# Kernel tuning notes

Measured on AMD Instinct MI355X. Metric: run time of the kernel, lower is better.

## Reference

```python
import jax, jax.numpy as jnp
import numpy as np

D_MODEL = 1024
N_LAYERS = 2
D_STATE = 16
D_CONV = 4
D_INNER = 2 * D_MODEL          # mamba expand=2
DT_RANK = 64                   # ceil(d_model/16)
EPS = 1e-5


def rmsnorm(x, w, eps=EPS):
    return x * jax.lax.rsqrt(jnp.mean(x * x, axis=-1, keepdims=True) + eps) * w


def silu(x):
    return x * jax.nn.sigmoid(x)


def selective_scan(u, dt, A, B, C, Dp):
    # u, dt: (b,l,d)  A: (d,n)  B,C: (b,l,n)  Dp: (d,)
    b, l, d = u.shape
    n = A.shape[1]

    def step(h, inp):
        u_t, dt_t, B_t, C_t = inp          # (b,d),(b,d),(b,n),(b,n)
        dA = jnp.exp(dt_t[..., None] * A)  # (b,d,n)
        h = dA * h + (dt_t * u_t)[..., None] * B_t[:, None, :]
        y = jnp.einsum('bdn,bn->bd', h, C_t)
        return h, y

    h0 = jnp.zeros((b, d, n), u.dtype)
    xs = (u.transpose(1, 0, 2), dt.transpose(1, 0, 2),
          B.transpose(1, 0, 2), C.transpose(1, 0, 2))
    _, ys = jax.lax.scan(step, h0, xs)
    return ys.transpose(1, 0, 2) + u * Dp


def mamba_mixer(x, in_w, conv_w, conv_b, xp_w, dt_w, dt_b, A_log, Dp, out_w):
    b, l, _ = x.shape
    xz = jnp.einsum('bld,ed->ble', x, in_w)        # (b,l,2*d_inner)
    xi, z = jnp.split(xz, 2, axis=-1)
    # depthwise causal conv1d, kernel D_CONV
    xp = jnp.pad(xi, ((0, 0), (D_CONV - 1, 0), (0, 0)))
    xc = conv_b + sum(xp[:, k:k + l, :] * conv_w[:, k] for k in range(D_CONV))
    xc = silu(xc)
    dbc = jnp.einsum('bld,ed->ble', xc, xp_w)      # (b,l,dt_rank+2n)
    dt_low = dbc[..., :DT_RANK]
    Bm = dbc[..., DT_RANK:DT_RANK + D_STATE]
    Cm = dbc[..., DT_RANK + D_STATE:]
    dt = jax.nn.softplus(jnp.einsum('blr,dr->bld', dt_low, dt_w) + dt_b)
    A = -jnp.exp(A_log)
    y = selective_scan(xc, dt, A, Bm, Cm, Dp)
    y = y * silu(z)
    return jnp.einsum('bld,od->blo', y, out_w)


def setup_inputs() -> dict:
    key = jax.random.key(0)
    ks = jax.random.split(key, 8)
    s = 0.02
    hidden_states = jax.random.normal(ks[0], (1, 2048, D_MODEL), jnp.float32)
    norm_w = jnp.ones((N_LAYERS, D_MODEL), jnp.float32)
    in_proj_w = jax.random.normal(ks[1], (N_LAYERS, 2 * D_INNER, D_MODEL), jnp.float32) * s
    conv_w = jax.random.normal(ks[2], (N_LAYERS, D_INNER, D_CONV), jnp.float32) * 0.2
    conv_b = jnp.zeros((N_LAYERS, D_INNER), jnp.float32)
    x_proj_w = jax.random.normal(ks[3], (N_LAYERS, DT_RANK + 2 * D_STATE, D_INNER), jnp.float32) * s
    dt_proj_w = jax.random.normal(ks[4], (N_LAYERS, D_INNER, DT_RANK), jnp.float32) * (DT_RANK ** -0.5)
    # softplus^{-1}(0.01) ~= -4.6 (mamba dt bias init regime)
    dt_proj_b = jnp.full((N_LAYERS, D_INNER), -4.6, jnp.float32) + \
        jax.random.normal(ks[5], (N_LAYERS, D_INNER), jnp.float32) * 0.1
    A_log = jnp.log(jnp.broadcast_to(
        jnp.arange(1, D_STATE + 1, dtype=jnp.float32), (N_LAYERS, D_INNER, D_STATE)))
    D_param = jnp.ones((N_LAYERS, D_INNER), jnp.float32)
    out_proj_w = jax.random.normal(ks[6], (N_LAYERS, D_MODEL, D_INNER), jnp.float32) * s
    norm_f_w = jnp.ones((D_MODEL,), jnp.float32)
    return {
        'hidden_states': hidden_states, 'norm_w': norm_w, 'in_proj_w': in_proj_w,
        'conv_w': conv_w, 'conv_b': conv_b, 'x_proj_w': x_proj_w,
        'dt_proj_w': dt_proj_w, 'dt_proj_b': dt_proj_b, 'A_log': A_log,
        'D_param': D_param, 'out_proj_w': out_proj_w, 'norm_f_w': norm_f_w,
    }


def reference(hidden_states, norm_w, in_proj_w, conv_w, conv_b, x_proj_w,
              dt_proj_w, dt_proj_b, A_log, D_param, out_proj_w, norm_f_w):
    h = hidden_states
    residual = None
    for i in range(N_LAYERS):
        # fused add + RMSNorm (prenorm): residual accumulates the stream
        residual = h if residual is None else h + residual
        hn = rmsnorm(residual, norm_w[i])
        h = mamba_mixer(hn, in_proj_w[i], conv_w[i], conv_b[i], x_proj_w[i],
                        dt_proj_w[i], dt_proj_b[i], A_log[i], D_param[i], out_proj_w[i])
    # final fused add + RMSNorm (prenorm=False)
    return rmsnorm(h + residual, norm_f_w)
```

## Files before the change

### kernel.cpp

```cpp
#include <hip/hip_runtime.h>
#include <math.h>

#define D_MODEL 1024
#define D_INNER 2048
#define DPROJ   96
#define DT_RANK 64
#define NSTATE  16
#define SEQ     2048
#define CL      16
#define NCH     (SEQ/CL)
#define SCAN_SEGS 4
#define SCAN_CPS  (NCH / SCAN_SEGS)
#define LOG2E   1.44269504088896340736f
#define TDC     ((size_t)SEQ * D_MODEL)

typedef unsigned short ushort_t;
typedef short v8s __attribute__((ext_vector_type(8)));
typedef unsigned short u8s __attribute__((ext_vector_type(8)));
typedef float v4f __attribute__((ext_vector_type(4)));
typedef __attribute__((address_space(3))) unsigned int as3_u32;
typedef __attribute__((address_space(1))) unsigned int as1_u32;

__device__ __forceinline__ float silu_f(float x) { return x / (1.f + expf(-x)); }

__device__ __forceinline__ ushort_t f2bf(float f) {
  union { float f; unsigned u; } x; x.f = f;
  unsigned r = x.u + 0x7fffu + ((x.u >> 16) & 1u);
  return (ushort_t)(r >> 16);
}
__device__ __forceinline__ float bf2f(ushort_t b) {
  union { unsigned u; float f; } x; x.u = ((unsigned)b) << 16; return x.f;
}

__device__ __forceinline__ void gl_lds16(const ushort_t* g, ushort_t* l) {
  __builtin_amdgcn_global_load_lds((const as1_u32*)g, (as3_u32*)l, 16, 0, 0);
}

__global__ __launch_bounds__(256) void addrms_kernel(
    const float* __restrict__ a, const ushort_t* __restrict__ p4,
    const float* __restrict__ b,
    const float* __restrict__ w, float* __restrict__ res_out,
    float* __restrict__ xnf, ushort_t* __restrict__ xnb) {
  int t = blockIdx.x;
  int tid = threadIdx.x;
  float v[4];
  float ss = 0.f;
#pragma unroll
  for (int j = 0; j < 4; ++j) {
    int dcol = tid + j * 256;
    size_t off = (size_t)t * D_MODEL + dcol;
    float x;
    if (p4) {
      x = bf2f(p4[off]) + bf2f(p4[off + TDC]) +
          bf2f(p4[off + 2 * TDC]) + bf2f(p4[off + 3 * TDC]);
    } else {
      x = a[off];
    }
    if (b) x += b[off];
    v[j] = x;
    ss += x * x;
  }
#pragma unroll
  for (int off = 32; off > 0; off >>= 1) ss += __shfl_down(ss, off);
  __shared__ float red[4];
  __shared__ float rmsv;
  int wid = tid >> 6, lane = tid & 63;
  if (lane == 0) red[wid] = ss;
  __syncthreads();
  if (tid == 0) {
    float s = red[0] + red[1] + red[2] + red[3];
    rmsv = rsqrtf(s / (float)D_MODEL + 1e-5f);
  }
  __syncthreads();
  float r = rmsv;
#pragma unroll
  for (int j = 0; j < 4; ++j) {
    int dcol = tid + j * 256;
    if (res_out) res_out[(size_t)t * D_MODEL + dcol] = v[j];
    float xn = v[j] * r * w[dcol];
    if (xnf) xnf[(size_t)t * D_MODEL + dcol] = xn;
    if (xnb) xnb[(size_t)t * D_MODEL + dcol] = f2bf(xn);
  }
}

__global__ __launch_bounds__(256) void f2bf_all_kernel(
    const float* __restrict__ s0, ushort_t* __restrict__ d0, int n0,
    const float* __restrict__ s1, ushort_t* __restrict__ d1, int n1,
    const float* __restrict__ s2, ushort_t* __restrict__ d2, int n2,
    const float* __restrict__ s3, ushort_t* __restrict__ d3, int n3) {
  int j = blockIdx.x * 256 + threadIdx.x;
  const float* s; ushort_t* d;
  if (j < n0) { s = s0; d = d0; }
  else {
    j -= n0;
    if (j < n1) { s = s1; d = d1; }
    else {
      j -= n1;
      if (j < n2) { s = s2; d = d2; }
      else {
        j -= n2;
        if (j >= n3) return;
        s = s3; d = d3;
      }
    }
  }
  float4 v = ((const float4*)s)[j];
  ushort4 o;
  o.x = f2bf(v.x); o.y = f2bf(v.y); o.z = f2bf(v.z); o.w = f2bf(v.w);
  ((ushort4*)d)[j] = o;
}

template <int SPLITK, bool CLAMPN, int EPI>
__global__ __launch_bounds__(256) void gemm_bt(
    const ushort_t* __restrict__ A, const ushort_t* __restrict__ B,
    void* __restrict__ Cv, const float* __restrict__ bias,
    const ushort_t* __restrict__ upack,
    int M, int N, int K, int lda, int ldb, int ldc) {
  __shared__ ushort_t As[2][128 * 32];
  __shared__ ushort_t Bs[2][128 * 32];
  int tid = threadIdx.x;

  int gx = gridDim.x, gy = gridDim.y;
  int nwg = gx * gy * gridDim.z;
  int phys = blockIdx.x + gx * (blockIdx.y + gy * blockIdx.z);
  int q = nwg >> 3, r = nwg & 7;
  int xcd = phys & 7, idx8 = phys >> 3;
  int lbid = (xcd < r ? xcd * (q + 1) : r * (q + 1) + (xcd - r) * q) + idx8;
  int bx = lbid % gx, by = (lbid / gx) % gy, bz = lbid / (gx * gy);

  int bm = by * 128;
  int bn = bx * 128;
  int kchunk = K / SPLITK;
  int k0 = bz * kchunk;
  int nk = kchunk / 32;

  int lane = tid & 63, wid = tid >> 6;
  int wr = wid >> 1, wc = wid & 1;
  int lr = lane & 15;
  int ko = (lane >> 4) * 8;

  int rs0 = wid * 16 + (lane >> 2);
  int segc = (lane & 3) * 8;

  auto stage = [&](int buf, int kt) {
#pragma unroll
    for (int s = 0; s < 2; ++s) {
      int r2 = s * 64 + rs0;
      int cc = kt + segc;
      gl_lds16(A + (size_t)(bm + r2) * lda + cc, &As[buf][s * 2048 + wid * 512]);
      int bc = bn + r2;
      if (CLAMPN) bc = min(bc, N - 1);
      gl_lds16(B + (size_t)bc * ldb + cc, &Bs[buf][s * 2048 + wid * 512]);
    }
  };

  v4f acc[4][4] = {};

  stage(0, k0);
  __syncthreads();
  int cur = 0;
  for (int it = 0; it < nk; ++it) {
    if (it + 1 < nk) stage(cur ^ 1, k0 + (it + 1) * 32);
    v8s a[4], b[4];
#pragma unroll
    for (int m = 0; m < 4; ++m)
      a[m] = *(const v8s*)&As[cur][(wr * 64 + m * 16 + lr) * 32 + ko];
#pragma unroll
    for (int n = 0; n < 4; ++n)
      b[n] = *(const v8s*)&Bs[cur][(wc * 64 + n * 16 + lr) * 32 + ko];
#pragma unroll
    for (int m = 0; m < 4; ++m)
#pragma unroll
      for (int n = 0; n < 4; ++n)
        acc[m][n] = __builtin_amdgcn_mfma_f32_16x16x32_bf16(a[m], b[n], acc[m][n], 0, 0, 0);
    __syncthreads();
    cur ^= 1;
  }

  float* Cf = (float*)Cv;
  ushort_t* Cb = (ushort_t*)Cv;
  unsigned* Cu = (unsigned*)Cv;
  size_t zoff = (SPLITK > 1) ? (size_t)bz * (size_t)M * (size_t)ldc : 0;

#pragma unroll
  for (int m = 0; m < 4; ++m) {
#pragma unroll
    for (int n = 0; n < 4; ++n) {
      int gc = bn + wc * 64 + n * 16 + lr;
      if (gc >= N) continue;
      int gr0 = bm + wr * 64 + m * 16 + (lane >> 4) * 4;
      float bv = (EPI == 1 || EPI == 3) ? bias[gc] : 0.f;
#pragma unroll
      for (int j = 0; j < 4; ++j) {
        float val = acc[m][n][j];
        size_t idx = zoff + (size_t)(gr0 + j) * ldc + gc;
        if (EPI == 0) {
          Cf[idx] = val;
        } else if (EPI == 1) {
          float x = val + bv;
          x = fmaxf(x, 0.f) + log1pf(expf(-fabsf(x)));
          Cb[idx] = f2bf(x);
        } else if (EPI == 2) {
          Cb[idx] = f2bf(val);
        } else {
          float x = val + bv;
          x = fmaxf(x, 0.f) + log1pf(expf(-fabsf(x)));
          Cu[idx] = (unsigned)f2bf(x) | ((unsigned)upack[idx] << 16);
        }
      }
    }
  }
}

__global__ __launch_bounds__(256) void convxproj_kernel(
    const ushort_t* __restrict__ xzb, const float* __restrict__ cw,
    const float* __restrict__ cb, const ushort_t* __restrict__ Bw,
    ushort_t* __restrict__ xcb, ushort_t* __restrict__ pkb) {
  __shared__ ushort_t As[128][136];
  __shared__ ushort_t Bs[2][128 * 32];
  int tid = threadIdx.x;
  int bm = blockIdx.y * 128;
  int c0s = blockIdx.z * 128;
  int k0 = c0s;

  {
    int quad = tid & 31;
    int tg = tid >> 5;
    int cc = c0s + quad * 4;
    int tbase = bm + tg * 16;
    float4 cbv = *(const float4*)&cb[cc];
    float4 wv[4];
#pragma unroll
    for (int i = 0; i < 4; ++i) wv[i] = *(const float4*)&cw[(cc + i) * 4];
    float rw[4][4];
#pragma unroll
    for (int p = 0; p < 3; ++p) {
      int ts = tbase - 3 + p;
      if (ts < 0) {
        rw[p][0] = rw[p][1] = rw[p][2] = rw[p][3] = 0.f;
      } else {
        ushort4 x = *(const ushort4*)&xzb[(size_t)ts * 4096 + cc];
        rw[p][0] = bf2f(x.x); rw[p][1] = bf2f(x.y);
        rw[p][2] = bf2f(x.z); rw[p][3] = bf2f(x.w);
      }
    }
#pragma unroll
    for (int j = 0; j < 16; ++j) {
      int t = tbase + j;
      {
        ushort4 x = *(const ushort4*)&xzb[(size_t)t * 4096 + cc];
        rw[(3 + j) & 3][0] = bf2f(x.x); rw[(3 + j) & 3][1] = bf2f(x.y);
        rw[(3 + j) & 3][2] = bf2f(x.z); rw[(3 + j) & 3][3] = bf2f(x.w);
      }
      float acc[4] = {cbv.x, cbv.y, cbv.z, cbv.w};
#pragma unroll
      for (int k = 0; k < 4; ++k) {
#pragma unroll
        for (int i = 0; i < 4; ++i)
          acc[i] = fmaf(rw[(j + k) & 3][i], ((const float*)&wv[i])[k], acc[i]);
      }
      ushort4 o;
      o.x = f2bf(silu_f(acc[0]));
      o.y = f2bf(silu_f(acc[1]));
      o.z = f2bf(silu_f(acc[2]));
      o.w = f2bf(silu_f(acc[3]));
      *(ushort4*)&As[tg * 16 + j][quad * 4] = o;
      *(ushort4*)&xcb[(size_t)t * D_INNER + cc] = o;
    }
  }

  int lane = tid & 63, wid = tid >> 6;
  int wr = wid >> 1, wc = wid & 1;
  int lr = lane & 15;
  int ko = (lane >> 4) * 8;
  int rs0 = wid * 16 + (lane >> 2);
  int segc = (lane & 3) * 8;

  auto stageB = [&](int buf, int it) {
#pragma unroll
    for (int s = 0; s < 2; ++s) {
      int r2 = s * 64 + rs0;
      int bc = min(r2, DPROJ - 1);
      int cc2 = k0 + it * 32 + segc;
      gl_lds16(Bw + (size_t)bc * D_INNER + cc2, &Bs[buf][s * 2048 + wid * 512]);
    }
  };

  v4f acc[4][4] = {};
  stageB(0, 0);
  __syncthreads();
  int cur = 0;
  for (int it = 0; it < 4; ++it) {
    if (it + 1 < 4) stageB(cur ^ 1, it + 1);
    v8s a[4], b[4];
#pragma unroll
    for (int m = 0; m < 4; ++m)
      a[m] = *(const v8s*)&As[wr * 64 + m * 16 + lr][it * 32 + ko];
#pragma unroll
    for (int n = 0; n < 4; ++n)
      b[n] = *(const v8s*)&Bs[cur][(wc * 64 + n * 16 + lr) * 32 + ko];
#pragma unroll
    for (int m = 0; m < 4; ++m)
#pragma unroll
      for (int n = 0; n < 4; ++n)
        acc[m][n] = __builtin_amdgcn_mfma_f32_16x16x32_bf16(a[m], b[n], acc[m][n], 0, 0, 0);
    __syncthreads();
    cur ^= 1;
  }

  size_t zoff = (size_t)blockIdx.z * (size_t)SEQ * DPROJ;
#pragma unroll
  for (int m = 0; m < 4; ++m) {
#pragma unroll
    for (int n = 0; n < 4; ++n) {
      int gc = wc * 64 + n * 16 + lr;
      if (gc >= DPROJ) continue;
      int gr0 = bm + wr * 64 + m * 16 + (lane >> 4) * 4;
#pragma unroll
      for (int j = 0; j < 4; ++j)
        pkb[zoff + (size_t)(gr0 + j) * DPROJ + gc] = f2bf(acc[m][n][j]);
    }
  }
}

__global__ __launch_bounds__(256) void reduceNb_kernel(
    const ushort_t* __restrict__ part, ushort_t* __restrict__ outb,
    int sz, int nparts) {
  int idx = blockIdx.x * 256 + threadIdx.x;
  if (idx >= sz) return;
  float s = 0.f;
  for (int p = 0; p < nparts; ++p) s += bf2f(part[idx + (size_t)p * sz]);
  outb[idx] = f2bf(s);
}

__global__ __launch_bounds__(256) void scan_passA_kernel(
    const unsigned* __restrict__ dtu, const ushort_t* __restrict__ dbcb,
    const float* __restrict__ A_log,
    ushort_t* __restrict__ aprodb, ushort_t* __restrict__ hendb) {
  __shared__ float Bsh[CL][16];
  int c = blockIdx.x;
  int d = blockIdx.y * 256 + threadIdx.x;
  int t0 = c * CL;
  {
    int j = threadIdx.x;
    if (j < CL * 4) {
      int r = j >> 2, col = (j & 3) * 4;
      ushort4 v = *(const ushort4*)&dbcb[(size_t)(t0 + r) * DPROJ + DT_RANK + col];
      Bsh[r][col]     = bf2f(v.x);
      Bsh[r][col + 1] = bf2f(v.y);
      Bsh[r][col + 2] = bf2f(v.z);
      Bsh[r][col + 3] = bf2f(v.w);
    }
  }
  float Av[NSTATE], h[NSTATE], ap[NSTATE];
#pragma unroll
  for (int n = 0; n < NSTATE; ++n) {
    Av[n] = -expf(A_log[(size_t)d * NSTATE + n]) * LOG2E;
    h[n] = 0.f;
    ap[n] = 1.f;
  }
  __syncthreads();
#pragma unroll 2
  for (int tt = 0; tt < CL; ++tt) {
    unsigned p = dtu[(size_t)(t0 + tt) * D_INNER + d];
    float dtv = bf2f((ushort_t)(p & 0xffffu));
    float uv  = bf2f((ushort_t)(p >> 16));
    float du = dtv * uv;
#pragma unroll
    for (int n = 0; n < NSTATE; ++n) {
      float dA = exp2f(dtv * Av[n]);
      h[n] = fmaf(dA, h[n], du * Bsh[tt][n]);
      ap[n] *= dA;
    }
  }
  size_t base = ((size_t)c * D_INNER + d) * NSTATE;
  u8s oa, ob, ha, hb;
#pragma unroll
  for (int n = 0; n < 8; ++n) {
    oa[n] = f2bf(ap[n]);     ob[n] = f2bf(ap[n + 8]);
    ha[n] = f2bf(h[n]);      hb[n] = f2bf(h[n + 8]);
  }
  *(u8s*)&aprodb[base] = oa;     *(u8s*)&aprodb[base + 8] = ob;
  *(u8s*)&hendb[base]  = ha;     *(u8s*)&hendb[base + 8]  = hb;
}

__global__ __launch_bounds__(256) void scan_passB_kernel(
    const ushort_t* __restrict__ aprodb, ushort_t* __restrict__ hendb) {
  int tid = threadIdx.x;
  int lane = tid & 63;
  int wave = tid >> 6;
  int seg = lane >> 4;
  int chain = blockIdx.x * 64 + wave * 16 + (lane & 15);
  const size_t stride = (size_t)D_INNER * NSTATE;
  float a[SCAN_CPS], e[SCAN_CPS];
  float P = 1.f, E = 0.f;
  int c0 = seg * SCAN_CPS;
#pragma unroll
  for (int j = 0; j < SCAN_CPS; ++j) {
    a[j] = bf2f(aprodb[(size_t)(c0 + j) * stride + chain]);
    e[j] = bf2f(hendb[(size_t)(c0 + j) * stride + chain]);
    E = fmaf(a[j], E, e[j]);
    P *= a[j];
  }
#pragma unroll
  for (int dstep = 1; dstep < SCAN_SEGS; dstep <<= 1) {
    float Pp = __shfl_up(P, dstep * 16);
    float Ep = __shfl_up(E, dstep * 16);
    if (seg >= dstep) { E = fmaf(P, Ep, E); P *= Pp; }
  }
  float Ex = __shfl_up(E, 16);
  if (seg == 0) Ex = 0.f;
  float h = Ex;
#pragma unroll
  for (int j = 0; j < SCAN_CPS; ++j) {
    hendb[(size_t)(c0 + j) * stride + chain] = f2bf(h);
    h = fmaf(a[j], h, e[j]);
  }
}

__global__ __launch_bounds__(256) void scan_passC_kernel(
    const unsigned* __restrict__ dtu, const ushort_t* __restrict__ dbcb,
    const float* __restrict__ A_log, const float* __restrict__ Dp,
    const ushort_t* __restrict__ xzb, const ushort_t* __restrict__ hinb,
    ushort_t* __restrict__ yb) {
  __shared__ float BCsh[CL][32];
  int c = blockIdx.x;
  int d = blockIdx.y * 256 + threadIdx.x;
  int t0 = c * CL;
  {
    int j = threadIdx.x;
    if (j < CL * 8) {
      int r = j >> 3, col = (j & 7) * 4;
      ushort4 v = *(const ushort4*)&dbcb[(size_t)(t0 + r) * DPROJ + DT_RANK + col];
      BCsh[r][col]     = bf2f(v.x);
      BCsh[r][col + 1] = bf2f(v.y);
      BCsh[r][col + 2] = bf2f(v.z);
      BCsh[r][col + 3] = bf2f(v.w);
    }
  }
  float Av[NSTATE], h[NSTATE];
  size_t base = ((size_t)c * D_INNER + d) * NSTATE;
  u8s h0 = *(const u8s*)&hinb[base];
  u8s h1 = *(const u8s*)&hinb[base + 8];
#pragma unroll
  for (int n = 0; n < NSTATE; ++n) {
    Av[n] = -expf(A_log[(size_t)d * NSTATE + n]) * LOG2E;
    h[n] = (n < 8) ? bf2f(h0[n & 7]) : bf2f(h1[n & 7]);
  }
  float Dv = Dp[d];
  __syncthreads();
#pragma unroll 2
  for (int tt = 0; tt < CL; ++tt) {
    unsigned p = dtu[(size_t)(t0 + tt) * D_INNER + d];
    float dtv = bf2f((ushort_t)(p & 0xffffu));
    float uv  = bf2f((ushort_t)(p >> 16));
    float du = dtv * uv;
    float yv = 0.f;
#pragma unroll
    for (int n = 0; n < NSTATE; ++n) {
      float dA = exp2f(dtv * Av[n]);
      h[n] = fmaf(dA, h[n], du * BCsh[tt][n]);
      yv = fmaf(h[n], BCsh[tt][16 + n], yv);
    }
    float zv = bf2f(xzb[(size_t)(t0 + tt) * 4096 + D_INNER + d]);
    yb[(size_t)(t0 + tt) * D_INNER + d] = f2bf((yv + uv * Dv) * silu_f(zv));
  }
}

extern "C" void kernel_launch(void* const* d_in, const int* in_sizes, int n_in,
                              void* d_out, int out_size, void* d_ws, size_t ws_size,
                              hipStream_t stream) {
  const float* h_in   = (const float*)d_in[0];
  const float* norm_w = (const float*)d_in[1];
  const float* in_w   = (const float*)d_in[2];
  const float* conv_w = (const float*)d_in[3];
  const float* conv_b = (const float*)d_in[4];
  const float* xp_w   = (const float*)d_in[5];
  const float* dt_w   = (const float*)d_in[6];
  const float* dt_b   = (const float*)d_in[7];
  const float* A_log  = (const float*)d_in[8];
  const float* Dp     = (const float*)d_in[9];
  const float* out_w  = (const float*)d_in[10];
  const float* normf  = (const float*)d_in[11];
  float* out = (float*)d_out;

  float* ws = (float*)d_ws;
  const size_t TD = (size_t)SEQ * D_MODEL;
  const size_t TI = (size_t)SEQ * D_INNER;
  const size_t ST = (size_t)NCH * D_INNER * NSTATE;
  const size_t DB = (size_t)SEQ * DPROJ;
  const size_t INW = (size_t)2 * D_INNER * D_MODEL;
  const size_t XPW = (size_t)DPROJ * D_INNER;
  const size_t DTW = (size_t)D_INNER * DT_RANK;
  const size_t OUW = (size_t)D_MODEL * D_INNER;

  float* res = ws; ws += TD;
  ushort_t* pkb = (ushort_t*)ws; ws += 2 * TD;
  unsigned* dtu = (unsigned*)ws; ws += TI;
  ushort_t* us = (ushort_t*)ws;
  ushort_t* aprodb = us;  us += ST;
  ushort_t* hendb  = us;  us += ST;
  ushort_t* hnb  = us;    us += TD;
  ushort_t* xzb  = us;    us += 2 * TI;
  ushort_t* xcb  = us;    us += TI;
  ushort_t* ybf  = us;    us += TI;
  ushort_t* dbcb = us;    us += DB;
  ushort_t* inwb = us;    us += 2 * INW;
  ushort_t* xpwb = us;    us += 2 * XPW;
  ushort_t* dtwb = us;    us += 2 * DTW;
  ushort_t* ouwb = us;    us += 2 * OUW;

  {
    int n0 = (int)(2 * INW / 4), n1 = (int)(2 * XPW / 4);
    int n2 = (int)(2 * DTW / 4), n3 = (int)(2 * OUW / 4);
    int tot = n0 + n1 + n2 + n3;
    f2bf_all_kernel<<<(tot + 255) / 256, 256, 0, stream>>>(
        in_w, inwb, n0, xp_w, xpwb, n1, dt_w, dtwb, n2, out_w, ouwb, n3);
  }

  for (int i = 0; i < 2; ++i) {
    addrms_kernel<<<SEQ, 256, 0, stream>>>(
        h_in, i == 0 ? nullptr : pkb,
        i == 0 ? nullptr : res,
        norm_w + (size_t)i * D_MODEL, res, nullptr, hnb);
    gemm_bt<1, false, 2><<<dim3(32, 16, 1), 256, 0, stream>>>(
        hnb, inwb + (size_t)i * INW, xzb, nullptr, nullptr,
        SEQ, 2 * D_INNER, D_MODEL, D_MODEL, D_MODEL, 2 * D_INNER);
    convxproj_kernel<<<dim3(1, 16, 16), 256, 0, stream>>>(
        xzb, conv_w + (size_t)i * D_INNER * 4, conv_b + (size_t)i * D_INNER,
        xpwb + (size_t)i * XPW, xcb, pkb);
    reduceNb_kernel<<<(DB + 255) / 256, 256, 0, stream>>>(pkb, dbcb, (int)DB, 16);
    gemm_bt<1, false, 3><<<dim3(16, 16, 1), 256, 0, stream>>>(
        dbcb, dtwb + (size_t)i * DTW, dtu, dt_b + (size_t)i * D_INNER, xcb,
        SEQ, D_INNER, DT_RANK, DPROJ, DT_RANK, D_INNER);
    scan_passA_kernel<<<dim3(NCH, D_INNER / 256), 256, 0, stream>>>(
        dtu, dbcb, A_log + (size_t)i * D_INNER * NSTATE, aprodb, hendb);
    scan_passB_kernel<<<(D_INNER * NSTATE) / 64, 256, 0, stream>>>(aprodb, hendb);
    scan_passC_kernel<<<dim3(NCH, D_INNER / 256), 256, 0, stream>>>(
        dtu, dbcb, A_log + (size_t)i * D_INNER * NSTATE,
        Dp + (size_t)i * D_INNER, xzb, hendb, ybf);
    gemm_bt<4, false, 2><<<dim3(8, 16, 4), 256, 0, stream>>>(
        ybf, ouwb + (size_t)i * OUW, pkb, nullptr, nullptr,
        SEQ, D_MODEL, D_INNER, D_INNER, D_INNER, D_MODEL);
  }
  addrms_kernel<<<SEQ, 256, 0, stream>>>(
      h_in, pkb, res, normf, nullptr, out, nullptr);
}
```

Baseline: 340.3 us.

## Split-K in_proj and out_proj GEMMs, reduce partials in consumers

The in_proj GEMM becomes split-K=2, writing two bf16 partial buffers that the conv and scan-C kernels sum when they read them. The out_proj GEMM goes from split-K 4 to 8, with addrms summing a variable number of partials. The dt GEMM no longer packs u with dt, so the scan kernels read dt and xc from separate arrays. This raises workgroup counts to fill more CUs, at the cost of extra partial-buffer traffic, a wider workspace, and an extra bf16 rounding per partial.

```diff
diff --git a/kernel.cpp b/kernel.cpp
--- a/kernel.cpp
+++ b/kernel.cpp
@@ -13,6 +13,7 @@
 #define SCAN_CPS  (NCH / SCAN_SEGS)
 #define LOG2E   1.44269504088896340736f
 #define TDC     ((size_t)SEQ * D_MODEL)
+#define XZP1    ((size_t)SEQ * 4096)
 
 typedef unsigned short ushort_t;
 typedef short v8s __attribute__((ext_vector_type(8)));
@@ -37,7 +38,7 @@
 }
 
 __global__ __launch_bounds__(256) void addrms_kernel(
-    const float* __restrict__ a, const ushort_t* __restrict__ p4,
+    const float* __restrict__ a, const ushort_t* __restrict__ pN, int nparts,
     const float* __restrict__ b,
     const float* __restrict__ w, float* __restrict__ res_out,
     float* __restrict__ xnf, ushort_t* __restrict__ xnb) {
@@ -50,9 +51,9 @@
     int dcol = tid + j * 256;
     size_t off = (size_t)t * D_MODEL + dcol;
     float x;
-    if (p4) {
-      x = bf2f(p4[off]) + bf2f(p4[off + TDC]) +
-          bf2f(p4[off + 2 * TDC]) + bf2f(p4[off + 3 * TDC]);
+    if (pN) {
+      x = 0.f;
+      for (int p = 0; p < nparts; ++p) x += bf2f(pN[off + (size_t)p * TDC]);
     } else {
       x = a[off];
     }
@@ -114,7 +115,6 @@
 __global__ __launch_bounds__(256) void gemm_bt(
     const ushort_t* __restrict__ A, const ushort_t* __restrict__ B,
     void* __restrict__ Cv, const float* __restrict__ bias,
-    const ushort_t* __restrict__ upack,
     int M, int N, int K, int lda, int ldb, int ldc) {
   __shared__ ushort_t As[2][128 * 32];
   __shared__ ushort_t Bs[2][128 * 32];
@@ -179,7 +179,6 @@
 
   float* Cf = (float*)Cv;
   ushort_t* Cb = (ushort_t*)Cv;
-  unsigned* Cu = (unsigned*)Cv;
   size_t zoff = (SPLITK > 1) ? (size_t)bz * (size_t)M * (size_t)ldc : 0;
 
 #pragma unroll
@@ -189,7 +188,7 @@
       int gc = bn + wc * 64 + n * 16 + lr;
       if (gc >= N) continue;
       int gr0 = bm + wr * 64 + m * 16 + (lane >> 4) * 4;
-      float bv = (EPI == 1 || EPI == 3) ? bias[gc] : 0.f;
+      float bv = (EPI == 1) ? bias[gc] : 0.f;
 #pragma unroll
       for (int j = 0; j < 4; ++j) {
         float val = acc[m][n][j];
@@ -200,12 +199,8 @@
           float x = val + bv;
           x = fmaxf(x, 0.f) + log1pf(expf(-fabsf(x)));
           Cb[idx] = f2bf(x);
-        } else if (EPI == 2) {
+        } else {
           Cb[idx] = f2bf(val);
-        } else {
-          float x = val + bv;
-          x = fmaxf(x, 0.f) + log1pf(expf(-fabsf(x)));
-          Cu[idx] = (unsigned)f2bf(x) | ((unsigned)upack[idx] << 16);
         }
       }
     }
@@ -213,7 +208,7 @@
 }
 
 __global__ __launch_bounds__(256) void convxproj_kernel(
-    const ushort_t* __restrict__ xzb, const float* __restrict__ cw,
+    const ushort_t* __restrict__ xzp, const float* __restrict__ cw,
     const float* __restrict__ cb, const ushort_t* __restrict__ Bw,
     ushort_t* __restrict__ xcb, ushort_t* __restrict__ pkb) {
   __shared__ ushort_t As[128][136];
@@ -239,18 +234,24 @@
       if (ts < 0) {
         rw[p][0] = rw[p][1] = rw[p][2] = rw[p][3] = 0.f;
       } else {
-        ushort4 x = *(const ushort4*)&xzb[(size_t)ts * 4096 + cc];
-        rw[p][0] = bf2f(x.x); rw[p][1] = bf2f(x.y);
-        rw[p][2] = bf2f(x.z); rw[p][3] = bf2f(x.w);
+        ushort4 x0 = *(const ushort4*)&xzp[(size_t)ts * 4096 + cc];
+        ushort4 x1 = *(const ushort4*)&xzp[XZP1 + (size_t)ts * 4096 + cc];
+        rw[p][0] = bf2f(x0.x) + bf2f(x1.x);
+        rw[p][1] = bf2f(x0.y) + bf2f(x1.y);
+        rw[p][2] = bf2f(x0.z) + bf2f(x1.z);
+        rw[p][3] = bf2f(x0.w) + bf2f(x1.w);
       }
     }
 #pragma unroll
     for (int j = 0; j < 16; ++j) {
       int t = tbase + j;
       {
-        ushort4 x = *(const ushort4*)&xzb[(size_t)t * 4096 + cc];
-        rw[(3 + j) & 3][0] = bf2f(x.x); rw[(3 + j) & 3][1] = bf2f(x.y);
-        rw[(3 + j) & 3][2] = bf2f(x.z); rw[(3 + j) & 3][3] = bf2f(x.w);
+        ushort4 x0 = *(const ushort4*)&xzp[(size_t)t * 4096 + cc];
+        ushort4 x1 = *(const ushort4*)&xzp[XZP1 + (size_t)t * 4096 + cc];
+        rw[(3 + j) & 3][0] = bf2f(x0.x) + bf2f(x1.x);
+        rw[(3 + j) & 3][1] = bf2f(x0.y) + bf2f(x1.y);
+        rw[(3 + j) & 3][2] = bf2f(x0.z) + bf2f(x1.z);
+        rw[(3 + j) & 3][3] = bf2f(x0.w) + bf2f(x1.w);
       }
       float acc[4] = {cbv.x, cbv.y, cbv.z, cbv.w};
 #pragma unroll
@@ -334,8 +335,8 @@
 }
 
 __global__ __launch_bounds__(256) void scan_passA_kernel(
-    const unsigned* __restrict__ dtu, const ushort_t* __restrict__ dbcb,
-    const float* __restrict__ A_log,
+    const ushort_t* __restrict__ dtbb, const ushort_t* __restrict__ xcb,
+    const ushort_t* __restrict__ dbcb, const float* __restrict__ A_log,
     ushort_t* __restrict__ aprodb, ushort_t* __restrict__ hendb) {
   __shared__ float Bsh[CL][16];
   int c = blockIdx.x;
@@ -362,9 +363,9 @@
   __syncthreads();
 #pragma unroll 2
   for (int tt = 0; tt < CL; ++tt) {
-    unsigned p = dtu[(size_t)(t0 + tt) * D_INNER + d];
-    float dtv = bf2f((ushort_t)(p & 0xffffu));
-    float uv  = bf2f((ushort_t)(p >> 16));
+    int t = t0 + tt;
+    float dtv = bf2f(dtbb[(size_t)t * D_INNER + d]);
+    float uv  = bf2f(xcb[(size_t)t * D_INNER + d]);
     float du = dtv * uv;
 #pragma unroll
     for (int n = 0; n < NSTATE; ++n) {
@@ -419,10 +420,10 @@
 }
 
 __global__ __launch_bounds__(256) void scan_passC_kernel(
-    const unsigned* __restrict__ dtu, const ushort_t* __restrict__ dbcb,
-    const float* __restrict__ A_log, const float* __restrict__ Dp,
-    const ushort_t* __restrict__ xzb, const ushort_t* __restrict__ hinb,
-    ushort_t* __restrict__ yb) {
+    const ushort_t* __restrict__ dtbb, const ushort_t* __restrict__ xcb,
+    const ushort_t* __restrict__ dbcb, const float* __restrict__ A_log,
+    const float* __restrict__ Dp, const ushort_t* __restrict__ xzp,
+    const ushort_t* __restrict__ hinb, ushort_t* __restrict__ yb) {
   __shared__ float BCsh[CL][32];
   int c = blockIdx.x;
   int d = blockIdx.y * 256 + threadIdx.x;
@@ -451,9 +452,9 @@
   __syncthreads();
 #pragma unroll 2
   for (int tt = 0; tt < CL; ++tt) {
-    unsigned p = dtu[(size_t)(t0 + tt) * D_INNER + d];
-    float dtv = bf2f((ushort_t)(p & 0xffffu));
-    float uv  = bf2f((ushort_t)(p >> 16));
+    int t = t0 + tt;
+    float dtv = bf2f(dtbb[(size_t)t * D_INNER + d]);
+    float uv  = bf2f(xcb[(size_t)t * D_INNER + d]);
     float du = dtv * uv;
     float yv = 0.f;
 #pragma unroll
@@ -462,8 +463,9 @@
       h[n] = fmaf(dA, h[n], du * BCsh[tt][n]);
       yv = fmaf(h[n], BCsh[tt][16 + n], yv);
     }
-    float zv = bf2f(xzb[(size_t)(t0 + tt) * 4096 + D_INNER + d]);
-    yb[(size_t)(t0 + tt) * D_INNER + d] = f2bf((yv + uv * Dv) * silu_f(zv));
+    size_t zi = (size_t)t * 4096 + D_INNER + d;
+    float zv = bf2f(xzp[zi]) + bf2f(xzp[XZP1 + zi]);
+    yb[(size_t)t * D_INNER + d] = f2bf((yv + uv * Dv) * silu_f(zv));
   }
 }
 
@@ -495,20 +497,20 @@
   const size_t OUW = (size_t)D_MODEL * D_INNER;
 
   float* res = ws; ws += TD;
-  ushort_t* pkb = (ushort_t*)ws; ws += 2 * TD;
-  unsigned* dtu = (unsigned*)ws; ws += TI;
   ushort_t* us = (ushort_t*)ws;
+  ushort_t* pkb    = us;  us += 8 * TD;
   ushort_t* aprodb = us;  us += ST;
   ushort_t* hendb  = us;  us += ST;
-  ushort_t* hnb  = us;    us += TD;
-  ushort_t* xzb  = us;    us += 2 * TI;
-  ushort_t* xcb  = us;    us += TI;
-  ushort_t* ybf  = us;    us += TI;
-  ushort_t* dbcb = us;    us += DB;
-  ushort_t* inwb = us;    us += 2 * INW;
-  ushort_t* xpwb = us;    us += 2 * XPW;
-  ushort_t* dtwb = us;    us += 2 * DTW;
-  ushort_t* ouwb = us;    us += 2 * OUW;
+  ushort_t* hnb    = us;  us += TD;
+  ushort_t* xzp    = us;  us += 4 * TI;
+  ushort_t* xcb    = us;  us += TI;
+  ushort_t* dtbb   = us;  us += TI;
+  ushort_t* ybf    = us;  us += TI;
+  ushort_t* dbcb   = us;  us += DB;
+  ushort_t* inwb   = us;  us += 2 * INW;
+  ushort_t* xpwb   = us;  us += 2 * XPW;
+  ushort_t* dtwb   = us;  us += 2 * DTW;
+  ushort_t* ouwb   = us;  us += 2 * OUW;
 
   {
     int n0 = (int)(2 * INW / 4), n1 = (int)(2 * XPW / 4);
@@ -520,29 +522,29 @@
 
   for (int i = 0; i < 2; ++i) {
     addrms_kernel<<<SEQ, 256, 0, stream>>>(
-        h_in, i == 0 ? nullptr : pkb,
+        h_in, i == 0 ? nullptr : pkb, 8,
         i == 0 ? nullptr : res,
         norm_w + (size_t)i * D_MODEL, res, nullptr, hnb);
-    gemm_bt<1, false, 2><<<dim3(32, 16, 1), 256, 0, stream>>>(
-        hnb, inwb + (size_t)i * INW, xzb, nullptr, nullptr,
+    gemm_bt<2, false, 2><<<dim3(32, 16, 2), 256, 0, stream>>>(
+        hnb, inwb + (size_t)i * INW, xzp, nullptr,
         SEQ, 2 * D_INNER, D_MODEL, D_MODEL, D_MODEL, 2 * D_INNER);
     convxproj_kernel<<<dim3(1, 16, 16), 256, 0, stream>>>(
-        xzb, conv_w + (size_t)i * D_INNER * 4, conv_b + (size_t)i * D_INNER,
+        xzp, conv_w + (size_t)i * D_INNER * 4, conv_b + (size_t)i * D_INNER,
         xpwb + (size_t)i * XPW, xcb, pkb);
     reduceNb_kernel<<<(DB + 255) / 256, 256, 0, stream>>>(pkb, dbcb, (int)DB, 16);
-    gemm_bt<1, false, 3><<<dim3(16, 16, 1), 256, 0, stream>>>(
-        dbcb, dtwb + (size_t)i * DTW, dtu, dt_b + (size_t)i * D_INNER, xcb,
+    gemm_bt<1, false, 1><<<dim3(16, 16, 1), 256, 0, stream>>>(
+        dbcb, dtwb + (size_t)i * DTW, dtbb, dt_b + (size_t)i * D_INNER,
         SEQ, D_INNER, DT_RANK, DPROJ, DT_RANK, D_INNER);
     scan_passA_kernel<<<dim3(NCH, D_INNER / 256), 256, 0, stream>>>(
-        dtu, dbcb, A_log + (size_t)i * D_INNER * NSTATE, aprodb, hendb);
+        dtbb, xcb, dbcb, A_log + (size_t)i * D_INNER * NSTATE, aprodb, hendb);
     scan_passB_kernel<<<(D_INNER * NSTATE) / 64, 256, 0, stream>>>(aprodb, hendb);
     scan_passC_kernel<<<dim3(NCH, D_INNER / 256), 256, 0, stream>>>(
-        dtu, dbcb, A_log + (size_t)i * D_INNER * NSTATE,
-        Dp + (size_t)i * D_INNER, xzb, hendb, ybf);
-    gemm_bt<4, false, 2><<<dim3(8, 16, 4), 256, 0, stream>>>(
-        ybf, ouwb + (size_t)i * OUW, pkb, nullptr, nullptr,
+        dtbb, xcb, dbcb, A_log + (size_t)i * D_INNER * NSTATE,
+        Dp + (size_t)i * D_INNER, xzp, hendb, ybf);
+    gemm_bt<8, false, 2><<<dim3(8, 16, 8), 256, 0, stream>>>(
+        ybf, ouwb + (size_t)i * OUW, pkb, nullptr,
         SEQ, D_MODEL, D_INNER, D_INNER, D_INNER, D_MODEL);
   }
   addrms_kernel<<<SEQ, 256, 0, stream>>>(
-      h_in, pkb, res, normf, nullptr, out, nullptr);
-}
+      h_in, pkb, 8, res, normf, nullptr, out, nullptr);
+}
```

Result: slower. 368.5 us (+8.3%).
